# Optimization experiments

Hardware: AMD Instinct MI355X
Metric: run time of the kernel (lower is better)

## Reference

```python
import jax, jax.numpy as jnp
import numpy as np

B, N, D = 2, 2048, 1024
H = 16
HD = D // H  # 64
N_CTX = 256


def setup_inputs() -> dict:
    key = jax.random.key(0)
    ks = jax.random.split(key, 10)
    x = jax.random.normal(ks[0], (B, N, D), dtype=jnp.float32)
    ctx_ppr = jax.random.uniform(ks[1], (N_CTX,), dtype=jnp.float32, minval=1e-4, maxval=1.0)
    ctx_trust = jax.random.uniform(ks[2], (N_CTX,), dtype=jnp.float32)
    attn_mask = jax.random.randint(ks[3], (N, N), 0, 2).astype(jnp.bool_)
    # parameters (nn.Linear convention: y = x @ W.T + b)
    s_in = 1.0 / np.sqrt(D)
    W_in = jax.random.uniform(ks[4], (3 * D, D), dtype=jnp.float32, minval=-s_in, maxval=s_in)
    b_in = jax.random.uniform(ks[5], (3 * D,), dtype=jnp.float32, minval=-s_in, maxval=s_in)
    W_out = jax.random.uniform(ks[6], (D, D), dtype=jnp.float32, minval=-s_in, maxval=s_in)
    b_out = jax.random.uniform(ks[7], (D,), dtype=jnp.float32, minval=-s_in, maxval=s_in)
    log_ppr_alpha = jnp.ones((1,), jnp.float32) * 0.1
    trust_scale = jnp.ones((1,), jnp.float32) * 0.1
    return {"x": x, "ctx_ppr": ctx_ppr, "ctx_trust": ctx_trust, "n_ctx": N_CTX,
            "attn_mask": attn_mask, "W_in": W_in, "b_in": b_in,
            "W_out": W_out, "b_out": b_out,
            "log_ppr_alpha": log_ppr_alpha, "trust_scale": trust_scale}


def reference(x, ctx_ppr, ctx_trust, n_ctx, attn_mask, W_in, b_in, W_out, b_out,
              log_ppr_alpha, trust_scale):
    Bx, Nx, Dx = x.shape
    scale = HD ** -0.5
    qkv = x @ W_in.T + b_in  # [B,N,3D]
    q, k, v = jnp.split(qkv, 3, axis=-1)
    q = q.reshape(Bx, Nx, H, HD).transpose(0, 2, 1, 3)  # [B,H,N,d]
    k = k.reshape(Bx, Nx, H, HD).transpose(0, 2, 1, 3)
    v = v.reshape(Bx, Nx, H, HD).transpose(0, 2, 1, 3)
    if n_ctx > 0:
        gate = jax.nn.sigmoid(trust_scale[0] * ctx_trust)  # [n_ctx]
        gate_full = jnp.concatenate([gate, jnp.ones(Nx - n_ctx, x.dtype)])
        v = v * gate_full[None, None, :, None]
    logits = jnp.einsum('bhqd,bhkd->bhqk', q, k) * scale
    if n_ctx > 0:
        bias = log_ppr_alpha[0] * jnp.log(jnp.clip(ctx_ppr, 1e-8, None))
        col_bias = jnp.concatenate([bias, jnp.zeros(Nx - n_ctx, x.dtype)])
        logits = logits + col_bias[None, None, None, :]
    logits = jnp.where(attn_mask[None, None, :, :], -jnp.inf, logits)
    weights = jax.nn.softmax(logits, axis=-1)
    out = jnp.einsum('bhqk,bhkd->bhqd', weights, v)
    out = out.transpose(0, 2, 1, 3).reshape(Bx, Nx, Dx)
    return out @ W_out.T + b_out
```

## Files before the change

### kernel.cpp

```cpp
#include <hip/hip_runtime.h>
#include <hip/hip_bf16.h>
#include <math.h>

#define B_   2
#define N_   2048
#define D_   1024
#define H_   16
#define TD_  3072
#define LOG2E 1.44269504088896340736f
#define SCALE_Q (0.125f * LOG2E)

typedef short  bf16x8 __attribute__((ext_vector_type(8)));
typedef _Float16 f16x8 __attribute__((ext_vector_type(8)));
typedef _Float16 f16x4 __attribute__((ext_vector_type(4)));
typedef float  f32x4  __attribute__((ext_vector_type(4)));
typedef float  f32x16 __attribute__((ext_vector_type(16)));

#define MFMA16(a, b, c)   __builtin_amdgcn_mfma_f32_16x16x32_bf16(a, b, c, 0, 0, 0)
#define MFMA32B(a, b, c)  __builtin_amdgcn_mfma_f32_32x32x16_bf16(a, b, c, 0, 0, 0)
#define MFMA32H(a, b, c)  __builtin_amdgcn_mfma_f32_32x32x16_f16(a, b, c, 0, 0, 0)

__device__ __forceinline__ ushort f2bf(float f) {
    union { float f; unsigned u; } v; v.f = f;
    unsigned r = (v.u + 0x7fffu + ((v.u >> 16) & 1u)) >> 16;
    return (ushort)r;
}
__device__ __forceinline__ unsigned pkrtz(float a, float b) {
    typedef __fp16 h2 __attribute__((ext_vector_type(2)));
    union { h2 h; unsigned u; } c;
    c.h = __builtin_amdgcn_cvt_pkrtz(a, b);
    return c.u;
}
__device__ __forceinline__ void async16(const void* g, void* l) {
    __builtin_amdgcn_global_load_lds(
        (const __attribute__((address_space(1))) unsigned*)g,
        (__attribute__((address_space(3))) unsigned*)l, 16, 0, 0);
}
__device__ __forceinline__ void plswap(unsigned &a, unsigned &b) {
    auto r = __builtin_amdgcn_permlane32_swap((int)a, (int)b, false, false);
    a = (unsigned)r[0]; b = (unsigned)r[1];
}

__global__ __launch_bounds__(256) void preprocess(
    const float* __restrict__ x, const float* __restrict__ W_in,
    const float* __restrict__ W_out, const float* __restrict__ ctx_ppr,
    const float* __restrict__ log_alpha, const int* __restrict__ n_ctx_p,
    const int* __restrict__ mask,
    ushort* __restrict__ xb, ushort* __restrict__ wib, ushort* __restrict__ wob,
    float* __restrict__ biasrow, unsigned* __restrict__ maskbits)
{
    const int J0 = 1048576, J1 = 786432, J2 = 262144, JM = 131072, JB = 2048;
    int t = blockIdx.x * 256 + threadIdx.x;
    if (t < J0 + J1 + J2) {
        const float* src; ushort* dst; int i = t;
        if (i < J0)           { src = x;      dst = xb;  }
        else if (i < J0 + J1) { i -= J0;      src = W_in;  dst = wib; }
        else                  { i -= J0 + J1; src = W_out; dst = wob; }
        float4 v = ((const float4*)src)[i];
        ushort4 o;
        o.x = f2bf(v.x); o.y = f2bf(v.y); o.z = f2bf(v.z); o.w = f2bf(v.w);
        ((ushort4*)dst)[i] = o;
    } else if (t < J0 + J1 + J2 + JM) {
        int i = t - (J0 + J1 + J2);
        const int4* m = (const int4*)(mask + (size_t)i * 32);
        unsigned bits = 0u;
        #pragma unroll
        for (int j = 0; j < 8; ++j) {
            int4 w = m[j];
            bits |= (w.x != 0 ? 1u : 0u) << (j * 4 + 0);
            bits |= (w.y != 0 ? 1u : 0u) << (j * 4 + 1);
            bits |= (w.z != 0 ? 1u : 0u) << (j * 4 + 2);
            bits |= (w.w != 0 ? 1u : 0u) << (j * 4 + 3);
        }
        maskbits[i] = bits;
    } else if (t < J0 + J1 + J2 + JM + JB) {
        int k = t - (J0 + J1 + J2 + JM);
        int nc = n_ctx_p[0];
        float bv = 0.f;
        if (k < nc) bv = log_alpha[0] * __log2f(fmaxf(ctx_ppr[k], 1e-8f));
        biasrow[k] = bv;
    }
}

template<int BCOL, int MODE>
__global__ __launch_bounds__(256) void gemm_bt(
    const ushort* __restrict__ A, const ushort* __restrict__ Bw,
    const float* __restrict__ bias, float* __restrict__ Cout,
    ushort* __restrict__ qkout, _Float16* __restrict__ vTout,
    int Ncol, int K,
    const float* __restrict__ ctx_trust, const float* __restrict__ trust_scale,
    const int* __restrict__ n_ctx_p)
{
    constexpr int NT = BCOL / 32;
    __shared__ ushort tA[128 * 32];
    __shared__ ushort tB[BCOL * 32];
    const int tid = threadIdx.x;
    const int lane = tid & 63, wv = tid >> 6;
    const int ln = lane & 15, kg = lane >> 4;
    const int rh = wv >> 1, ch = wv & 1;
    const int row0 = blockIdx.y * 128, col0 = blockIdx.x * BCOL;

    int offA[4], offB[NT];
    #pragma unroll
    for (int i = 0; i < 4; ++i) {
        int ra = rh * 64 + i * 16 + ln;
        offA[i] = ra * 32 + ((kg ^ ((ra >> 1) & 3)) << 3);
    }
    #pragma unroll
    for (int i = 0; i < NT; ++i) {
        int rb = ch * (BCOL / 2) + i * 16 + ln;
        offB[i] = rb * 32 + ((kg ^ ((rb >> 1) & 3)) << 3);
    }
    f32x4 acc[4][NT];
    #pragma unroll
    for (int i = 0; i < 4; ++i)
        #pragma unroll
        for (int j = 0; j < NT; ++j) acc[i][j] = (f32x4){0.f, 0.f, 0.f, 0.f};

    for (int kt = 0; kt < K; kt += 32) {
        __syncthreads();
        #pragma unroll
        for (int r2 = 0; r2 < 2; ++r2) {
            int g = r2 * 256 + tid;
            int row = g >> 2;
            int srck = ((g & 3) ^ ((row >> 1) & 3)) << 3;
            async16(A + (size_t)(row0 + row) * K + kt + srck, &tA[g * 8]);
        }
        #pragma unroll
        for (int r2 = 0; r2 < BCOL / 64; ++r2) {
            int g = r2 * 256 + tid;
            int row = g >> 2;
            int srck = ((g & 3) ^ ((row >> 1) & 3)) << 3;
            async16(Bw + (size_t)(col0 + row) * K + kt + srck, &tB[g * 8]);
        }
        __syncthreads();
        bf16x8 af[4], bfr[NT];
        #pragma unroll
        for (int i = 0; i < 4; ++i)  af[i]  = *(const bf16x8*)&tA[offA[i]];
        #pragma unroll
        for (int i = 0; i < NT; ++i) bfr[i] = *(const bf16x8*)&tB[offB[i]];
        #pragma unroll
        for (int mt = 0; mt < 4; ++mt)
            #pragma unroll
            for (int nt = 0; nt < NT; ++nt)
                acc[mt][nt] = MFMA16(af[mt], bfr[nt], acc[mt][nt]);
    }

    const int nctx = n_ctx_p ? n_ctx_p[0] : 0;
    const float ts = trust_scale ? trust_scale[0] : 0.f;
    #pragma unroll
    for (int nt = 0; nt < NT; ++nt) {
        int col = col0 + ch * (BCOL / 2) + nt * 16 + ln;
        float bv = bias[col];
        #pragma unroll
        for (int mt = 0; mt < 4; ++mt) {
            int rbase = row0 + rh * 64 + mt * 16 + kg * 4;
            f32x4 a = acc[mt][nt];
            if (MODE == 0) {
                #pragma unroll
                for (int reg = 0; reg < 4; ++reg)
                    Cout[(size_t)(rbase + reg) * Ncol + col] = a[reg] + bv;
            } else {
                if (col < D_) {
                    #pragma unroll
                    for (int reg = 0; reg < 4; ++reg)
                        qkout[(size_t)(rbase + reg) * 2048 + col] =
                            f2bf((a[reg] + bv) * SCALE_Q);
                } else if (col < 2 * D_) {
                    #pragma unroll
                    for (int reg = 0; reg < 4; ++reg)
                        qkout[(size_t)(rbase + reg) * 2048 + col] = f2bf(a[reg] + bv);
                } else {
                    int vc = col - 2 * D_;
                    int hh = vc >> 6, dim = vc & 63;
                    int bb = rbase >> 11, nbase = rbase & (N_ - 1);
                    ushort4 o;
                    #pragma unroll
                    for (int reg = 0; reg < 4; ++reg) {
                        float v = a[reg] + bv;
                        int n = nbase + reg;
                        if (n < nctx) {
                            float g = 1.f / (1.f + __expf(-ts * ctx_trust[n]));
                            v *= g;
                        }
                        _Float16 hv = (_Float16)v;
                        ((ushort*)&o)[reg] = *(ushort*)&hv;
                    }
                    *(ushort4*)&vTout[((size_t)(bb * 16 + hh) * 64 + dim) * 2048 + nbase] = o;
                }
            }
        }
    }
}

__global__ __launch_bounds__(256) void attn(
    const ushort* __restrict__ qkb,
    const _Float16* __restrict__ vT,
    const unsigned* __restrict__ maskbits,
    const float* __restrict__ biasrow,
    const int* __restrict__ n_ctx_p,
    _Float16* __restrict__ op0,
    _Float16* __restrict__ op1,
    float* __restrict__ lpart)
{
    __shared__ ushort   Kt[2][64 * 64];
    __shared__ _Float16 Vt[2][64 * 64];
    const int tid = threadIdx.x;
    const int lane = tid & 63, wv = tid >> 6;
    const int q31 = lane & 31, hi = lane >> 5;
    const int b = blockIdx.y >> 4, h = blockIdx.y & 15;
    const int q0w = blockIdx.x * 128 + wv * 32;
    const int kh = blockIdx.z;
    const int kbase = kh << 10;
    const int nctx = n_ctx_p[0];

    bf16x8 qf[4];
    {
        const ushort* qrow = qkb + (size_t)(b * N_ + q0w + q31) * 2048 + h * 64;
        #pragma unroll
        for (int ks = 0; ks < 4; ++ks)
            qf[ks] = *(const bf16x8*)(qrow + ks * 16 + hi * 8);
    }
    const size_t kgbase = (size_t)(b * N_ + kbase) * 2048 + 1024 + h * 64;
    const _Float16* vbase = vT + (size_t)((b * 16 + h) * 64) * 2048 + kbase;

    f32x16 O[2];
    O[0] = (f32x16)(0.f); O[1] = (f32x16)(0.f);
    float lrun = 0.f;

    {
        #pragma unroll
        for (int r2 = 0; r2 < 2; ++r2) {
            int g = r2 * 256 + tid; int row = g >> 3; int sg = (g & 7) ^ (row & 7);
            async16(qkb + kgbase + (size_t)row * 2048 + sg * 8, &Kt[0][g * 8]);
        }
        #pragma unroll
        for (int r2 = 0; r2 < 2; ++r2) {
            int g = r2 * 256 + tid; int row = g >> 3; int sg = (g & 7) ^ (row & 7);
            async16(vbase + (size_t)row * 2048 + sg * 8, &Vt[0][g * 8]);
        }
    }

    const int swz = q31 & 7;
    for (int ci = 0; ci < 16; ++ci) {
        const int c0 = ci * 64;
        __syncthreads();
        if (ci < 15) {
            const int c1 = c0 + 64, nb = (ci + 1) & 1;
            #pragma unroll
            for (int r2 = 0; r2 < 2; ++r2) {
                int g = r2 * 256 + tid; int row = g >> 3; int sg = (g & 7) ^ (row & 7);
                async16(qkb + kgbase + (size_t)(c1 + row) * 2048 + sg * 8, &Kt[nb][g * 8]);
            }
            #pragma unroll
            for (int r2 = 0; r2 < 2; ++r2) {
                int g = r2 * 256 + tid; int row = g >> 3; int sg = (g & 7) ^ (row & 7);
                async16(vbase + (size_t)row * 2048 + c1 + sg * 8, &Vt[nb][g * 8]);
            }
        }
        const ushort*   KT = Kt[ci & 1];
        const _Float16* VT = Vt[ci & 1];

        f32x16 S[2];
        S[0] = (f32x16)(0.f); S[1] = (f32x16)(0.f);
        #pragma unroll
        for (int t = 0; t < 2; ++t) {
            const int rbase = (t * 32 + q31) * 64;
            #pragma unroll
            for (int ks = 0; ks < 4; ++ks) {
                bf16x8 kf = *(const bf16x8*)&KT[rbase + (((ks * 2 + hi) ^ swz) << 3)];
                S[t] = MFMA32B(kf, qf[ks], S[t]);
            }
        }

        uint2 mw = *(const uint2*)&maskbits[(size_t)(q0w + q31) * 64 + (kbase >> 5) + ci * 2];
        unsigned msh[2] = { mw.x >> (hi * 4), mw.y >> (hi * 4) };
        unsigned pk[2][8];
        float lsum = 0.f;
        const int c0g = kbase + c0;
        const bool has_bias = (c0g < nctx);
        #pragma unroll
        for (int t = 0; t < 2; ++t) {
            float p[16];
            #pragma unroll
            for (int g = 0; g < 4; ++g) {
                f32x4 bb = (f32x4){0.f, 0.f, 0.f, 0.f};
                if (has_bias)
                    bb = *(const f32x4*)&biasrow[c0g + t * 32 + g * 8 + hi * 4];
                #pragma unroll
                for (int r = 0; r < 4; ++r) {
                    const int reg = g * 4 + r;
                    const int br = r + 8 * g;
                    float s = S[t][reg] + bb[r] - 4.f;
                    s = ((msh[t] >> br) & 1u) ? -1e30f : s;
                    p[reg] = __builtin_exp2f(s);
                }
            }
            float l0 = (p[0] + p[1]) + (p[2] + p[3]);
            float l1 = (p[4] + p[5]) + (p[6] + p[7]);
            float l2 = (p[8] + p[9]) + (p[10] + p[11]);
            float l3 = (p[12] + p[13]) + (p[14] + p[15]);
            lsum += (l0 + l1) + (l2 + l3);
            #pragma unroll
            for (int i = 0; i < 8; ++i)
                pk[t][i] = pkrtz(p[2 * i], p[2 * i + 1]);
        }
        lrun += lsum;

        #pragma unroll
        for (int ks = 0; ks < 4; ++ks) {
            const int t = ks >> 1, lo4 = (ks & 1) * 4;
            unsigned w0 = pk[t][lo4 + 0], w1 = pk[t][lo4 + 1];
            unsigned w2 = pk[t][lo4 + 2], w3 = pk[t][lo4 + 3];
            plswap(w0, w2);
            plswap(w1, w3);
            union { f16x8 v; unsigned u[4]; } frag;
            frag.u[0] = w0; frag.u[1] = w1;
            frag.u[2] = w2; frag.u[3] = w3;
            #pragma unroll
            for (int t2 = 0; t2 < 2; ++t2) {
                const int vb = (t2 * 32 + q31) * 64;
                union { f16x8 v; int4 i; } vf;
                vf.i = *(const int4*)&VT[vb + (((ks * 2 + hi) ^ swz) << 3)];
                O[t2] = MFMA32H(vf.v, frag.v, O[t2]);
            }
        }
    }

    float l = lrun + __shfl_xor(lrun, 32);
    float inv = 1.f / l;
    _Float16* orow = (kh ? op1 : op0)
                   + (size_t)(b * N_ + q0w + q31) * 1024 + h * 64;
    #pragma unroll
    for (int t = 0; t < 2; ++t)
        #pragma unroll
        for (int g = 0; g < 4; ++g) {
            ushort4 o;
            #pragma unroll
            for (int r = 0; r < 4; ++r) {
                _Float16 hv = (_Float16)(O[t][g * 4 + r] * inv);
                ((ushort*)&o)[r] = *(ushort*)&hv;
            }
            *(ushort4*)&orow[t * 32 + g * 8 + hi * 4] = o;
        }
    if (hi == 0)
        lpart[(kh << 16) + (b * 16 + h) * 2048 + q0w + q31] = l;
}

__global__ __launch_bounds__(256) void combine(
    const _Float16* __restrict__ op0, const _Float16* __restrict__ op1,
    const float* __restrict__ lpart, ushort* __restrict__ attb)
{
    int t = blockIdx.x * 256 + threadIdx.x;
    size_t idx = (size_t)t * 4;
    int col = (int)(idx & 1023);
    int row = (int)(idx >> 10);
    int h = col >> 6;
    int b = row >> 11, q = row & 2047;
    int lidx = (b * 16 + h) * 2048 + q;
    float l0 = lpart[lidx], l1 = lpart[65536 + lidx];
    float inv = 1.f / (l0 + l1);
    float w0 = l0 * inv, w1 = l1 * inv;
    f16x4 a0 = *(const f16x4*)(op0 + idx);
    f16x4 a1 = *(const f16x4*)(op1 + idx);
    ushort4 o;
    #pragma unroll
    for (int r = 0; r < 4; ++r)
        ((ushort*)&o)[r] = f2bf((float)a0[r] * w0 + (float)a1[r] * w1);
    *(ushort4*)(attb + idx) = o;
}

extern "C" void kernel_launch(void* const* d_in, const int* in_sizes, int n_in,
                              void* d_out, int out_size, void* d_ws, size_t ws_size,
                              hipStream_t stream)
{
    const float* x         = (const float*)d_in[0];
    const float* ctx_ppr   = (const float*)d_in[1];
    const float* ctx_trust = (const float*)d_in[2];
    const int*   n_ctx_p   = (const int*)d_in[3];
    const int*   attn_mask = (const int*)d_in[4];
    const float* W_in      = (const float*)d_in[5];
    const float* b_in      = (const float*)d_in[6];
    const float* W_out     = (const float*)d_in[7];
    const float* b_out     = (const float*)d_in[8];
    const float* log_alpha = (const float*)d_in[9];
    const float* trust_sc  = (const float*)d_in[10];
    float* out = (float*)d_out;

    char* ws = (char*)d_ws;
    ushort*    xb       = (ushort*)ws;    ws += (size_t)4096 * 1024 * 2;
    ushort*    wib      = (ushort*)ws;    ws += (size_t)3072 * 1024 * 2;
    ushort*    wob      = (ushort*)ws;    ws += (size_t)1024 * 1024 * 2;
    ushort*    qkb      = (ushort*)ws;    ws += (size_t)4096 * 2048 * 2;
    _Float16*  vT       = (_Float16*)ws;  ws += (size_t)2048 * 2048 * 2;
    ushort*    attbuf   = (ushort*)ws;    ws += (size_t)4096 * 1024 * 2;
    float*     biasrow  = (float*)ws;     ws += 2048 * 4;
    unsigned*  maskbits = (unsigned*)ws;  ws += (size_t)2048 * 64 * 4;

    _Float16* op0   = (_Float16*)xb;
    _Float16* op1   = (_Float16*)attbuf;
    float*    lpart = (float*)wib;

    hipLaunchKernelGGL(preprocess, dim3(8712), dim3(256), 0, stream,
                       x, W_in, W_out, ctx_ppr, log_alpha, n_ctx_p, attn_mask,
                       xb, wib, wob, biasrow, maskbits);

    hipLaunchKernelGGL((gemm_bt<128, 1>), dim3(24, 32), dim3(256), 0, stream,
                       xb, wib, b_in, (float*)nullptr, qkb, vT, TD_, 1024,
                       ctx_trust, trust_sc, n_ctx_p);

    hipLaunchKernelGGL(attn, dim3(16, 32, 2), dim3(256), 0, stream,
                       qkb, vT, maskbits, biasrow, n_ctx_p, op0, op1, lpart);

    hipLaunchKernelGGL(combine, dim3(4096), dim3(256), 0, stream,
                       op0, op1, lpart, attbuf);

    hipLaunchKernelGGL((gemm_bt<64, 0>), dim3(16, 32), dim3(256), 0, stream,
                       attbuf, wob, b_out, out, (ushort*)nullptr, (_Float16*)nullptr,
                       1024, 1024, ctx_trust, trust_sc, n_ctx_p);
}
```

Baseline: 269.8 us.

## Triple-buffer K tiles with explicit vmcnt waits and prefetch mask bits

The attention kernel moves K tiles to a three-stage LDS ring prefetched two chunks ahead, while V stays double-buffered. Explicit s_waitcnt/s_barrier replace __syncthreads, and the next chunk's mask word is loaded one iteration early. The per-tile S computation is interleaved with the PV MFMAs to cut live registers, and launch bounds request 4 blocks per CU. The aim is to hide global load latency and raise occupancy, at the cost of extra LDS and fragile hand-counted vmcnt values.

```diff
diff --git a/kernel.cpp b/kernel.cpp
--- a/kernel.cpp
+++ b/kernel.cpp
@@ -193,7 +193,7 @@
     }
 }
 
-__global__ __launch_bounds__(256) void attn(
+__global__ __launch_bounds__(256, 4) void attn(
     const ushort* __restrict__ qkb,
     const _Float16* __restrict__ vT,
     const unsigned* __restrict__ maskbits,
@@ -203,7 +203,7 @@
     _Float16* __restrict__ op1,
     float* __restrict__ lpart)
 {
-    __shared__ ushort   Kt[2][64 * 64];
+    __shared__ ushort   Kt[3][64 * 64];
     __shared__ _Float16 Vt[2][64 * 64];
     const int tid = threadIdx.x;
     const int lane = tid & 63, wv = tid >> 6;
@@ -223,75 +223,88 @@
     }
     const size_t kgbase = (size_t)(b * N_ + kbase) * 2048 + 1024 + h * 64;
     const _Float16* vbase = vT + (size_t)((b * 16 + h) * 64) * 2048 + kbase;
+    const unsigned* mrow = maskbits + (size_t)(q0w + q31) * 64 + (kbase >> 5);
+
+    int goff[2], ldso[2];
+    #pragma unroll
+    for (int r2 = 0; r2 < 2; ++r2) {
+        int g = r2 * 256 + tid, row = g >> 3, sg = (g & 7) ^ (row & 7);
+        goff[r2] = row * 2048 + sg * 8;
+        ldso[r2] = g * 8;
+    }
 
     f32x16 O[2];
     O[0] = (f32x16)(0.f); O[1] = (f32x16)(0.f);
     float lrun = 0.f;
 
+    uint2 mcur = *(const uint2*)&mrow[0];
+    asm volatile("" ::: "memory");
     {
-        #pragma unroll
-        for (int r2 = 0; r2 < 2; ++r2) {
-            int g = r2 * 256 + tid; int row = g >> 3; int sg = (g & 7) ^ (row & 7);
-            async16(qkb + kgbase + (size_t)row * 2048 + sg * 8, &Kt[0][g * 8]);
-        }
-        #pragma unroll
-        for (int r2 = 0; r2 < 2; ++r2) {
-            int g = r2 * 256 + tid; int row = g >> 3; int sg = (g & 7) ^ (row & 7);
-            async16(vbase + (size_t)row * 2048 + sg * 8, &Vt[0][g * 8]);
-        }
+        const ushort* gp0 = qkb + kgbase;
+        #pragma unroll
+        for (int r2 = 0; r2 < 2; ++r2) async16(gp0 + goff[r2], &Kt[0][ldso[r2]]);
+        const _Float16* vp = vbase;
+        #pragma unroll
+        for (int r2 = 0; r2 < 2; ++r2) async16(vp + goff[r2], &Vt[0][ldso[r2]]);
+        const ushort* gp1 = qkb + kgbase + (size_t)(64 * 2048);
+        #pragma unroll
+        for (int r2 = 0; r2 < 2; ++r2) async16(gp1 + goff[r2], &Kt[1][ldso[r2]]);
     }
 
     const int swz = q31 & 7;
+    int kb = 0;
+    #pragma unroll 1
     for (int ci = 0; ci < 16; ++ci) {
-        const int c0 = ci * 64;
-        __syncthreads();
+        asm volatile("s_barrier" ::: "memory");
+        uint2 mnext = mcur;
         if (ci < 15) {
-            const int c1 = c0 + 64, nb = (ci + 1) & 1;
-            #pragma unroll
-            for (int r2 = 0; r2 < 2; ++r2) {
-                int g = r2 * 256 + tid; int row = g >> 3; int sg = (g & 7) ^ (row & 7);
-                async16(qkb + kgbase + (size_t)(c1 + row) * 2048 + sg * 8, &Kt[nb][g * 8]);
-            }
-            #pragma unroll
-            for (int r2 = 0; r2 < 2; ++r2) {
-                int g = r2 * 256 + tid; int row = g >> 3; int sg = (g & 7) ^ (row & 7);
-                async16(vbase + (size_t)row * 2048 + c1 + sg * 8, &Vt[nb][g * 8]);
-            }
-        }
-        const ushort*   KT = Kt[ci & 1];
+            mnext = *(const uint2*)&mrow[(ci + 1) * 2];
+            asm volatile("" ::: "memory");
+            const _Float16* vp = vbase + (ci + 1) * 64;
+            #pragma unroll
+            for (int r2 = 0; r2 < 2; ++r2)
+                async16(vp + goff[r2], &Vt[(ci + 1) & 1][ldso[r2]]);
+        }
+        if (ci < 14) {
+            int nb = kb + 2; if (nb >= 3) nb -= 3;
+            const ushort* gp = qkb + kgbase + (size_t)(ci + 2) * (64 * 2048);
+            #pragma unroll
+            for (int r2 = 0; r2 < 2; ++r2)
+                async16(gp + goff[r2], &Kt[nb][ldso[r2]]);
+        }
+        if (ci < 14)       asm volatile("s_waitcnt vmcnt(7)" ::: "memory");
+        else if (ci == 14) asm volatile("s_waitcnt vmcnt(5)" ::: "memory");
+        else               asm volatile("s_waitcnt vmcnt(0)" ::: "memory");
+        asm volatile("s_barrier" ::: "memory");
+
+        const ushort*   KT = Kt[kb];
         const _Float16* VT = Vt[ci & 1];
-
-        f32x16 S[2];
-        S[0] = (f32x16)(0.f); S[1] = (f32x16)(0.f);
+        const int c0g = kbase + ci * 64;
+        const bool has_bias = (c0g < nctx);
+        unsigned msh[2] = { mcur.x >> (hi * 4), mcur.y >> (hi * 4) };
+        float lsum = 0.f;
+
         #pragma unroll
         for (int t = 0; t < 2; ++t) {
+            f32x16 S = (f32x16)(0.f);
             const int rbase = (t * 32 + q31) * 64;
             #pragma unroll
             for (int ks = 0; ks < 4; ++ks) {
                 bf16x8 kf = *(const bf16x8*)&KT[rbase + (((ks * 2 + hi) ^ swz) << 3)];
-                S[t] = MFMA32B(kf, qf[ks], S[t]);
+                S = MFMA32B(kf, qf[ks], S);
             }
-        }
-
-        uint2 mw = *(const uint2*)&maskbits[(size_t)(q0w + q31) * 64 + (kbase >> 5) + ci * 2];
-        unsigned msh[2] = { mw.x >> (hi * 4), mw.y >> (hi * 4) };
-        unsigned pk[2][8];
-        float lsum = 0.f;
-        const int c0g = kbase + c0;
-        const bool has_bias = (c0g < nctx);
-        #pragma unroll
-        for (int t = 0; t < 2; ++t) {
             float p[16];
             #pragma unroll
             for (int g = 0; g < 4; ++g) {
-                f32x4 bb = (f32x4){0.f, 0.f, 0.f, 0.f};
+                f32x4 bb;
                 if (has_bias)
                     bb = *(const f32x4*)&biasrow[c0g + t * 32 + g * 8 + hi * 4];
                 #pragma unroll
                 for (int r = 0; r < 4; ++r) {
                     const int reg = g * 4 + r;
                     const int br = r + 8 * g;
-                    float s = S[t][reg] + bb[r] - 4.f;
+                    float s = S[reg] - 4.f;
+                    if (has_bias) s += bb[r];
                     s = ((msh[t] >> br) & 1u) ? -1e30f : s;
                     p[reg] = __builtin_exp2f(s);
                 }
@@ -301,30 +314,33 @@
             float l2 = (p[8] + p[9]) + (p[10] + p[11]);
             float l3 = (p[12] + p[13]) + (p[14] + p[15]);
             lsum += (l0 + l1) + (l2 + l3);
+            unsigned pk[8];
             #pragma unroll
             for (int i = 0; i < 8; ++i)
-                pk[t][i] = pkrtz(p[2 * i], p[2 * i + 1]);
+                pk[i] = pkrtz(p[2 * i], p[2 * i + 1]);
+
+            #pragma unroll
+            for (int kss = 0; kss < 2; ++kss) {
+                const int ks = 2 * t + kss, lo4 = kss * 4;
+                unsigned w0 = pk[lo4 + 0], w1 = pk[lo4 + 1];
+                unsigned w2 = pk[lo4 + 2], w3 = pk[lo4 + 3];
+                plswap(w0, w2);
+                plswap(w1, w3);
+                union { f16x8 v; unsigned u[4]; } frag;
+                frag.u[0] = w0; frag.u[1] = w1;
+                frag.u[2] = w2; frag.u[3] = w3;
+                #pragma unroll
+                for (int t2 = 0; t2 < 2; ++t2) {
+                    const int vb = (t2 * 32 + q31) * 64;
+                    union { f16x8 v; int4 i4; } vf;
+                    vf.i4 = *(const int4*)&VT[vb + (((ks * 2 + hi) ^ swz) << 3)];
+                    O[t2] = MFMA32H(vf.v, frag.v, O[t2]);
+                }
+            }
         }
         lrun += lsum;
-
-        #pragma unroll
-        for (int ks = 0; ks < 4; ++ks) {
-            const int t = ks >> 1, lo4 = (ks & 1) * 4;
-            unsigned w0 = pk[t][lo4 + 0], w1 = pk[t][lo4 + 1];
-            unsigned w2 = pk[t][lo4 + 2], w3 = pk[t][lo4 + 3];
-            plswap(w0, w2);
-            plswap(w1, w3);
-            union { f16x8 v; unsigned u[4]; } frag;
-            frag.u[0] = w0; frag.u[1] = w1;
-            frag.u[2] = w2; frag.u[3] = w3;
-            #pragma unroll
-            for (int t2 = 0; t2 < 2; ++t2) {
-                const int vb = (t2 * 32 + q31) * 64;
-                union { f16x8 v; int4 i; } vf;
-                vf.i = *(const int4*)&VT[vb + (((ks * 2 + hi) ^ swz) << 3)];
-                O[t2] = MFMA32H(vf.v, frag.v, O[t2]);
-            }
-        }
+        mcur = mnext;
+        kb = kb + 1; if (kb >= 3) kb -= 3;
     }
 
     float l = lrun + __shfl_xor(lrun, 32);
```

Result: no change. 269.6 us (-0.1%).
